# Optimization experiments

Measured on AMD Instinct MI355X. Metric: run time of the kernel, lower is better.

The kernel has to match this reference:

```python
import jax, jax.numpy as jnp
import numpy as np

B, N, E, H = 8, 1024, 768, 12
HD = E // H  # head_dim = 64
EPS = 1e-5


def setup_inputs() -> dict:
    key = jax.random.key(0)
    ks = jax.random.split(key, 3)
    x = jax.random.normal(ks[0], (B, N, E), dtype=jnp.float32)
    # Packed in-projection like torch nn.MultiheadAttention (in_proj_weight [3E, E])
    w_qkv = jax.random.normal(ks[1], (3 * E, E), dtype=jnp.float32) * (1.0 / np.sqrt(E))
    b_qkv = jnp.zeros((3 * E,), dtype=jnp.float32)
    w_out = jax.random.normal(ks[2], (E, E), dtype=jnp.float32) * (1.0 / np.sqrt(E))
    b_out = jnp.zeros((E,), dtype=jnp.float32)
    ln_g = jnp.ones((E,), dtype=jnp.float32)
    ln_b = jnp.zeros((E,), dtype=jnp.float32)
    return {"x": x, "ln_g": ln_g, "ln_b": ln_b, "w_qkv": w_qkv,
            "b_qkv": b_qkv, "w_out": w_out, "b_out": b_out}


def reference(x, ln_g, ln_b, w_qkv, b_qkv, w_out, b_out):
    # LayerNorm over last dim (eps=1e-5, elementwise affine)
    mu = jnp.mean(x, axis=-1, keepdims=True)
    var = jnp.mean(jnp.square(x - mu), axis=-1, keepdims=True)
    xn = (x - mu) * jax.lax.rsqrt(var + EPS) * ln_g + ln_b

    # Packed QKV projection: torch does x @ in_proj_weight.T + in_proj_bias
    qkv = jnp.einsum('bne,fe->bnf', xn, w_qkv) + b_qkv  # [B, N, 3E]
    q, k, v = jnp.split(qkv, 3, axis=-1)
    # Split heads -> [B, H, N, HD]
    q = q.reshape(B, N, H, HD).transpose(0, 2, 1, 3)
    k = k.reshape(B, N, H, HD).transpose(0, 2, 1, 3)
    v = v.reshape(B, N, H, HD).transpose(0, 2, 1, 3)

    scale = 1.0 / np.sqrt(HD)
    scores = jnp.einsum('bhqd,bhkd->bhqk', q * scale, k)  # [B, H, N, N]
    attn = jax.nn.softmax(scores, axis=-1)
    # (attn_dropout=0.0; need_weights=True forces this manual path in torch,
    #  averaged weights attn.mean(axis=1) are computed but not returned here
    #  since return_attention_map defaults to False)
    ctx = jnp.einsum('bhqk,bhkd->bhqd', attn, v)  # [B, H, N, HD]
    ctx = ctx.transpose(0, 2, 1, 3).reshape(B, N, E)

    out = jnp.einsum('bne,fe->bnf', ctx, w_out) + b_out  # out_proj
    return out
```

## Files before the change

kernel.cpp:

```cpp
#include <hip/hip_runtime.h>
#include <hip/hip_bf16.h>
#include <stdint.h>

#define B_ 8
#define N_ 1024
#define E_ 768
#define H_ 12
#define HD_ 64
#define M_ (B_ * N_)

typedef __attribute__((ext_vector_type(8))) short bf8_t;
typedef __attribute__((ext_vector_type(4))) float f4_t;
typedef __attribute__((ext_vector_type(16))) float f16_t;

__device__ __forceinline__ unsigned short f2bf(float f) {
  unsigned u = __builtin_bit_cast(unsigned, f);
  unsigned r = (u + 0x7fffu + ((u >> 16) & 1u)) >> 16;
  return (unsigned short)r;
}

__device__ __forceinline__ unsigned cvt_pk_bf16(float lo, float hi) {
  unsigned r;
  asm("v_cvt_pk_bf16_f32 %0, %1, %2" : "=v"(r) : "v"(lo), "v"(hi));
  return r;
}

__device__ __forceinline__ float exp2_hw(float x) {
  float r;
  asm("v_exp_f32 %0, %1" : "=v"(r) : "v"(x));
  return r;
}

__device__ __forceinline__ void load_lds16(const void* g, void* l) {
  __builtin_amdgcn_global_load_lds(
      (__attribute__((address_space(1))) void*)(g),
      (__attribute__((address_space(3))) void*)(l), 16, 0, 0);
}

#define WAITV(N)                                        \
  asm volatile("s_waitcnt vmcnt(" #N ")" ::: "memory"); \
  __builtin_amdgcn_sched_barrier(0);                    \
  __builtin_amdgcn_s_barrier();                         \
  __builtin_amdgcn_sched_barrier(0);

#define BAR2()                          \
  __builtin_amdgcn_sched_barrier(0);    \
  __builtin_amdgcn_s_barrier();         \
  __builtin_amdgcn_sched_barrier(0);

__device__ __forceinline__ int swz(int row) {
  return ((row ^ (row >> 3)) & 7) << 3;
}

#define F3(a, b, c) fmaxf(fmaxf((a), (b)), (c))

__global__ void k_cast_bf16(const float* __restrict__ in,
                            unsigned short* __restrict__ out, int n4) {
  int i = blockIdx.x * blockDim.x + threadIdx.x;
  if (i < n4) {
    float4 v = ((const float4*)in)[i];
    ushort4 o;
    o.x = f2bf(v.x); o.y = f2bf(v.y); o.z = f2bf(v.z); o.w = f2bf(v.w);
    ((ushort4*)out)[i] = o;
  }
}

__global__ __launch_bounds__(192) void k_ln(const float* __restrict__ x,
                                            const float* __restrict__ g,
                                            const float* __restrict__ bta,
                                            unsigned short* __restrict__ xn) {
  int row = blockIdx.x;
  int t = threadIdx.x;
  float4 v = ((const float4*)(x + (size_t)row * E_))[t];
  float s = v.x + v.y + v.z + v.w;
  float s2 = v.x * v.x + v.y * v.y + v.z * v.z + v.w * v.w;
  for (int off = 32; off; off >>= 1) {
    s += __shfl_xor(s, off, 64);
    s2 += __shfl_xor(s2, off, 64);
  }
  __shared__ float red[6];
  int lane = t & 63, wv = t >> 6;
  if (lane == 0) { red[wv] = s; red[3 + wv] = s2; }
  __syncthreads();
  s = red[0] + red[1] + red[2];
  s2 = red[3] + red[4] + red[5];
  float mu = s * (1.0f / E_);
  float var = s2 * (1.0f / E_) - mu * mu;
  float rstd = rsqrtf(var + 1e-5f);
  float4 gg = ((const float4*)g)[t];
  float4 bb = ((const float4*)bta)[t];
  ushort4 o;
  o.x = f2bf((v.x - mu) * rstd * gg.x + bb.x);
  o.y = f2bf((v.y - mu) * rstd * gg.y + bb.y);
  o.z = f2bf((v.z - mu) * rstd * gg.z + bb.z);
  o.w = f2bf((v.w - mu) * rstd * gg.w + bb.w);
  ((ushort4*)(xn + (size_t)row * E_))[t] = o;
}

template <int EPI>
__global__ __launch_bounds__(256) void k_gemm_bt(
    const unsigned short* __restrict__ A,
    const unsigned short* __restrict__ W,
    const float* __restrict__ bias,
    unsigned short* __restrict__ oQ, unsigned short* __restrict__ oK,
    unsigned short* __restrict__ oVt, float* __restrict__ oF,
    int K, int Nf) {
  __shared__ unsigned short Al[2][128 * 64];
  __shared__ unsigned short Bl[2][128 * 64];
  const int nbx = Nf >> 7;
  const int nwg = nbx << 6;
  const int orig = blockIdx.y * nbx + blockIdx.x;
  const int id = (orig & 7) * (nwg >> 3) + (orig >> 3);
  const int n0 = (id % nbx) * 128, m0 = (id / nbx) * 128;
  const int tid = threadIdx.x;
  const int lane = tid & 63, wv = tid >> 6;
  const int wr = wv >> 1, wc = wv & 1;
  const int g = lane >> 4, l15 = lane & 15;
  f4_t acc[4][4] = {};

  auto stage = [&](int k0, int buf) {
#pragma unroll
    for (int i = 0; i < 4; ++i) {
      int e = (i * 256 + tid) * 8;
      int r = e >> 6;
      int c = (e & 63) ^ swz(r);
      load_lds16(A + (size_t)(m0 + r) * K + (k0 + c), &Al[buf][e]);
      load_lds16(W + (size_t)(n0 + r) * K + (k0 + c), &Bl[buf][e]);
    }
  };

  stage(0, 0);
  __syncthreads();
  int cur = 0;

  for (int k0 = 0; k0 < K; k0 += 64) {
    if (k0 + 64 < K) stage(k0 + 64, cur ^ 1);
    const unsigned short* Ac = Al[cur];
    const unsigned short* Bc = Bl[cur];
#pragma unroll
    for (int kk = 0; kk < 2; ++kk) {
      bf8_t af[4], bfr[4];
#pragma unroll
      for (int mi = 0; mi < 4; ++mi) {
        int ar = wr * 64 + mi * 16 + l15;
        af[mi] = *(const bf8_t*)&Ac[(ar * 64 + kk * 32 + g * 8) ^ swz(ar)];
      }
#pragma unroll
      for (int ni = 0; ni < 4; ++ni) {
        int br = wc * 64 + ni * 16 + l15;
        bfr[ni] = *(const bf8_t*)&Bc[(br * 64 + kk * 32 + g * 8) ^ swz(br)];
      }
#pragma unroll
      for (int mi = 0; mi < 4; ++mi)
#pragma unroll
        for (int ni = 0; ni < 4; ++ni)
          acc[mi][ni] = __builtin_amdgcn_mfma_f32_16x16x32_bf16(
              af[mi], bfr[ni], acc[mi][ni], 0, 0, 0);
    }
    __syncthreads();
    cur ^= 1;
  }

#pragma unroll
  for (int mi = 0; mi < 4; ++mi) {
#pragma unroll
    for (int ni = 0; ni < 4; ++ni) {
      int f = n0 + wc * 64 + ni * 16 + l15;
      float bs = bias[f];
#pragma unroll
      for (int i = 0; i < 4; ++i) {
        int m = m0 + wr * 64 + mi * 16 + g * 4 + i;
        float val = acc[mi][ni][i] + bs;
        if (EPI == 0) {
          int bb = m >> 10, n = m & 1023;
          int which = f / E_;
          int e2 = f - which * E_;
          int h = e2 >> 6, d = e2 & 63;
          size_t qk = (((size_t)bb * H_ + h) * N_ + n) * HD_ + d;
          if (which == 0) oQ[qk] = f2bf(val * 0.1803368801f);
          else if (which == 1) oK[qk] = f2bf(val);
          else oVt[(((size_t)bb * H_ + h) * HD_ + d) * N_ + n] = f2bf(val);
        } else {
          oF[(size_t)m * E_ + f] = val;
        }
      }
    }
  }
}

__global__ __launch_bounds__(256, 3) void k_attn(
    const unsigned short* __restrict__ Q,
    const unsigned short* __restrict__ Kb,
    const unsigned short* __restrict__ Vt,
    unsigned short* __restrict__ ctx) {
  __shared__ unsigned short Kl[2][64 * 64];
  __shared__ unsigned short Vl[2][64 * 64];
  const int bh = blockIdx.x;
  const int qt = blockIdx.y;
  const int tid = threadIdx.x;
  const int lane = tid & 63, wv = tid >> 6;
  const int q5 = lane & 31, hi = lane >> 5;

  const unsigned short* Qp =
      Q + ((size_t)bh * N_ + qt * 128 + wv * 32 + q5) * HD_;
  bf8_t qf[4];
#pragma unroll
  for (int s = 0; s < 4; ++s)
    qf[s] = *(const bf8_t*)&Qp[s * 16 + hi * 8];

  f16_t o0 = {}, o1 = {};
  float mrow = -1e30f, lrow = 0.f;
  const unsigned short* Kbase = Kb + (size_t)bh * N_ * HD_;
  const unsigned short* Vbase = Vt + (size_t)bh * HD_ * N_;

  auto stage = [&](int t, int buf) {
#pragma unroll
    for (int i = 0; i < 2; ++i) {
      int e = (i * 256 + tid) * 8;
      int r = e >> 6;
      int c = (e & 63) ^ swz(r);
      load_lds16(Kbase + (size_t)(t * 64 + r) * HD_ + c, &Kl[buf][e]);
      load_lds16(Vbase + (size_t)r * N_ + (t * 64 + c), &Vl[buf][e]);
    }
  };

  stage(0, 0);
  stage(1, 1);

  for (int t = 0; t < 16; ++t) {
    const int cur = t & 1;
    if (t + 1 < 16) { WAITV(4); } else { WAITV(0); }
    const unsigned short* Klc = Kl[cur];
    const unsigned short* Vlc = Vl[cur];

    f16_t s0 = {}, s1 = {};
    __builtin_amdgcn_s_setprio(1);
#pragma unroll
    for (int s = 0; s < 4; ++s) {
      int doff = s * 16 + hi * 8;
      bf8_t k0 = *(const bf8_t*)&Klc[(q5 * 64 + doff) ^ swz(q5)];
      bf8_t k1 = *(const bf8_t*)&Klc[((32 + q5) * 64 + doff) ^ swz(32 + q5)];
      s0 = __builtin_amdgcn_mfma_f32_32x32x16_bf16(k0, qf[s], s0, 0, 0, 0);
      s1 = __builtin_amdgcn_mfma_f32_32x32x16_bf16(k1, qf[s], s1, 0, 0, 0);
    }
    __builtin_amdgcn_s_setprio(0);

    float v0 = F3(s0[0], s0[1], s0[2]),   v1 = F3(s0[3], s0[4], s0[5]);
    float v2 = F3(s0[6], s0[7], s0[8]),   v3 = F3(s0[9], s0[10], s0[11]);
    float v4 = F3(s0[12], s0[13], s0[14]), v5 = F3(s0[15], s1[0], s1[1]);
    float v6 = F3(s1[2], s1[3], s1[4]),   v7 = F3(s1[5], s1[6], s1[7]);
    float v8 = F3(s1[8], s1[9], s1[10]),  v9 = F3(s1[11], s1[12], s1[13]);
    float w0 = F3(v0, v1, v2), w1 = F3(v3, v4, v5);
    float w2 = F3(v6, v7, v8), w3 = F3(v9, s1[14], s1[15]);
    float mx = fmaxf(F3(w0, w1, w2), w3);

    if (!__all(mx - mrow <= 8.0f)) {
      float Mx = fmaxf(mx, __shfl_xor(mx, 32, 64));
      float mnew = fmaxf(mrow, Mx);
      float al = exp2_hw(mrow - mnew);
      lrow *= al;
#pragma unroll
      for (int r = 0; r < 16; ++r) { o0[r] *= al; o1[r] *= al; }
      mrow = mnew;
    }

    float p[32];
#pragma unroll
    for (int r = 0; r < 16; ++r) p[r] = exp2_hw(s0[r] - mrow);
#pragma unroll
    for (int r = 0; r < 16; ++r) p[16 + r] = exp2_hw(s1[r] - mrow);
    float acc0 = 0.f, acc1 = 0.f, acc2 = 0.f, acc3 = 0.f;
#pragma unroll
    for (int r = 0; r < 8; ++r) {
      acc0 += p[r]; acc1 += p[8 + r]; acc2 += p[16 + r]; acc3 += p[24 + r];
    }
    lrow += (acc0 + acc1) + (acc2 + acc3);

    unsigned pj[4][4];
#pragma unroll
    for (int s = 0; s < 4; ++s) {
      unsigned Ax = cvt_pk_bf16(p[8 * s + 0], p[8 * s + 1]);
      unsigned Cx = cvt_pk_bf16(p[8 * s + 2], p[8 * s + 3]);
      unsigned Ex = cvt_pk_bf16(p[8 * s + 4], p[8 * s + 5]);
      unsigned Fx = cvt_pk_bf16(p[8 * s + 6], p[8 * s + 7]);
      asm volatile("v_permlane32_swap_b32 %0, %1" : "+v"(Ax), "+v"(Ex));
      asm volatile("v_permlane32_swap_b32 %0, %1" : "+v"(Cx), "+v"(Fx));
      pj[s][0] = Ax; pj[s][1] = Cx; pj[s][2] = Ex; pj[s][3] = Fx;
    }

    __builtin_amdgcn_s_setprio(1);
#pragma unroll
    for (int s = 0; s < 4; ++s) {
      int koff = s * 16 + hi * 8;
      bf8_t pb;
      *(uint4*)&pb = *(uint4*)&pj[s][0];
      bf8_t vv0 = *(const bf8_t*)&Vlc[(q5 * 64 + koff) ^ swz(q5)];
      bf8_t vv1 = *(const bf8_t*)&Vlc[((32 + q5) * 64 + koff) ^ swz(32 + q5)];
      o0 = __builtin_amdgcn_mfma_f32_32x32x16_bf16(vv0, pb, o0, 0, 0, 0);
      o1 = __builtin_amdgcn_mfma_f32_32x32x16_bf16(vv1, pb, o1, 0, 0, 0);
    }
    __builtin_amdgcn_s_setprio(0);

    BAR2();
    if (t + 2 < 16) stage(t + 2, cur);
  }

  lrow += __shfl_xor(lrow, 32, 64);
  float rinv = 1.0f / lrow;

  unsigned short* Ol = &Kl[0][0] + wv * 2048;
#pragma unroll
  for (int f = 0; f < 2; ++f) {
#pragma unroll
    for (int r = 0; r < 16; r += 2) {
      int d = (r & 3) + 8 * (r >> 2) + 4 * hi + 32 * f;
      float lo = (f ? o1[r] : o0[r]) * rinv;
      float hi2 = (f ? o1[r + 1] : o0[r + 1]) * rinv;
      unsigned pk = cvt_pk_bf16(lo, hi2);
      *(unsigned*)&Ol[q5 * 64 + (d ^ ((q5 & 7) << 3))] = pk;
    }
  }
  asm volatile("s_waitcnt lgkmcnt(0)" ::: "memory");
  __builtin_amdgcn_sched_barrier(0);

  const int bb = bh / H_, h = bh - bb * H_;
  const int qq = lane >> 1;
#pragma unroll
  for (int k = 0; k < 4; ++k) {
    int c = (lane & 1) * 4 + k;
    bf8_t val = *(const bf8_t*)&Ol[qq * 64 + ((c * 8) ^ ((qq & 7) << 3))];
    unsigned short* dst = ctx +
        ((size_t)bb * N_ + qt * 128 + wv * 32 + qq) * E_ + h * HD_ + c * 8;
    *(bf8_t*)dst = val;
  }
}

extern "C" void kernel_launch(void* const* d_in, const int* in_sizes, int n_in,
                              void* d_out, int out_size, void* d_ws, size_t ws_size,
                              hipStream_t stream) {
  const float* x     = (const float*)d_in[0];
  const float* ln_g  = (const float*)d_in[1];
  const float* ln_b  = (const float*)d_in[2];
  const float* w_qkv = (const float*)d_in[3];
  const float* b_qkv = (const float*)d_in[4];
  const float* w_out = (const float*)d_in[5];
  const float* b_out = (const float*)d_in[6];
  float* out = (float*)d_out;

  char* ws = (char*)d_ws;
  const size_t SZ = (size_t)M_ * E_ * 2;
  unsigned short* xn    = (unsigned short*)(ws);
  unsigned short* qb    = (unsigned short*)(ws + SZ);
  unsigned short* kbuf  = (unsigned short*)(ws + 2 * SZ);
  unsigned short* vtb   = (unsigned short*)(ws + 3 * SZ);
  unsigned short* ctx   = (unsigned short*)(ws + 4 * SZ);
  unsigned short* wqkvb = (unsigned short*)(ws + 5 * SZ);
  unsigned short* woutb = (unsigned short*)(ws + 5 * SZ + (size_t)3 * E_ * E_ * 2);

  int n1 = 3 * E_ * E_ / 4;
  k_cast_bf16<<<(n1 + 255) / 256, 256, 0, stream>>>(w_qkv, wqkvb, n1);
  int n2 = E_ * E_ / 4;
  k_cast_bf16<<<(n2 + 255) / 256, 256, 0, stream>>>(w_out, woutb, n2);

  k_ln<<<M_, 192, 0, stream>>>(x, ln_g, ln_b, xn);

  k_gemm_bt<0><<<dim3(18, 64), 256, 0, stream>>>(xn, wqkvb, b_qkv, qb, kbuf, vtb,
                                                 nullptr, E_, 3 * E_);
  k_attn<<<dim3(96, 8), 256, 0, stream>>>(qb, kbuf, vtb, ctx);
  k_gemm_bt<1><<<dim3(6, 64), 256, 0, stream>>>(ctx, woutb, b_out, nullptr, nullptr,
                                                nullptr, out, E_, E_);
}
```

Measured before the change: 137.6 us.

## Use 256x128 GEMM tiles with 512 threads and triple-buffered LDS pipeline

Both projection GEMMs now use 512-thread workgroups covering 256x128 output tiles, with a three-stage LDS ring buffer. Wait counts on the vector memory counter replace full syncthreads, so loads stay two stages ahead of the MFMA work. MFMA sections are wrapped in raised wave priority. This aims to hide global-load latency and reuse each staged W tile across more rows. In exchange it uses much more LDS (about 144KB) and limits occupancy to one block per CU. It also halves the grid, which hurts the 6x32 out-projection launch in particular.

```diff
diff --git a/kernel.cpp b/kernel.cpp
--- a/kernel.cpp
+++ b/kernel.cpp
@@ -98,20 +98,20 @@
 }
 
 template <int EPI>
-__global__ __launch_bounds__(256) void k_gemm_bt(
+__global__ __launch_bounds__(512, 1) void k_gemm_deep(
     const unsigned short* __restrict__ A,
     const unsigned short* __restrict__ W,
     const float* __restrict__ bias,
     unsigned short* __restrict__ oQ, unsigned short* __restrict__ oK,
-    unsigned short* __restrict__ oVt, float* __restrict__ oF,
-    int K, int Nf) {
-  __shared__ unsigned short Al[2][128 * 64];
-  __shared__ unsigned short Bl[2][128 * 64];
+    unsigned short* __restrict__ oVt, float* __restrict__ oF, int Nf) {
+  __shared__ unsigned short Al[3][256 * 64];
+  __shared__ unsigned short Bl[3][128 * 64];
+  const int K = 768;
   const int nbx = Nf >> 7;
-  const int nwg = nbx << 6;
+  const int nwg = nbx << 5;
   const int orig = blockIdx.y * nbx + blockIdx.x;
   const int id = (orig & 7) * (nwg >> 3) + (orig >> 3);
-  const int n0 = (id % nbx) * 128, m0 = (id / nbx) * 128;
+  const int n0 = (id % nbx) * 128, m0 = (id / nbx) * 256;
   const int tid = threadIdx.x;
   const int lane = tid & 63, wv = tid >> 6;
   const int wr = wv >> 1, wc = wv & 1;
@@ -121,20 +121,29 @@
   auto stage = [&](int k0, int buf) {
 #pragma unroll
     for (int i = 0; i < 4; ++i) {
-      int e = (i * 256 + tid) * 8;
+      int e = (i * 512 + tid) * 8;
       int r = e >> 6;
       int c = (e & 63) ^ swz(r);
       load_lds16(A + (size_t)(m0 + r) * K + (k0 + c), &Al[buf][e]);
+    }
+#pragma unroll
+    for (int i = 0; i < 2; ++i) {
+      int e = (i * 512 + tid) * 8;
+      int r = e >> 6;
+      int c = (e & 63) ^ swz(r);
       load_lds16(W + (size_t)(n0 + r) * K + (k0 + c), &Bl[buf][e]);
     }
   };
 
   stage(0, 0);
-  __syncthreads();
-  int cur = 0;
-
-  for (int k0 = 0; k0 < K; k0 += 64) {
-    if (k0 + 64 < K) stage(k0 + 64, cur ^ 1);
+  stage(64, 1);
+  stage(128, 2);
+
+  for (int t = 0; t < 12; ++t) {
+    const int cur = t % 3;
+    if (t + 2 < 12)      { WAITV(12); }
+    else if (t + 1 < 12) { WAITV(6); }
+    else                 { WAITV(0); }
     const unsigned short* Ac = Al[cur];
     const unsigned short* Bc = Bl[cur];
 #pragma unroll
@@ -150,15 +159,17 @@
         int br = wc * 64 + ni * 16 + l15;
         bfr[ni] = *(const bf8_t*)&Bc[(br * 64 + kk * 32 + g * 8) ^ swz(br)];
       }
+      __builtin_amdgcn_s_setprio(1);
 #pragma unroll
       for (int mi = 0; mi < 4; ++mi)
 #pragma unroll
         for (int ni = 0; ni < 4; ++ni)
           acc[mi][ni] = __builtin_amdgcn_mfma_f32_16x16x32_bf16(
               af[mi], bfr[ni], acc[mi][ni], 0, 0, 0);
-    }
-    __syncthreads();
-    cur ^= 1;
+      __builtin_amdgcn_s_setprio(0);
+    }
+    BAR2();
+    if (t + 3 < 12) stage((t + 3) << 6, cur);
   }
 
 #pragma unroll
@@ -364,9 +375,9 @@
 
   k_ln<<<M_, 192, 0, stream>>>(x, ln_g, ln_b, xn);
 
-  k_gemm_bt<0><<<dim3(18, 64), 256, 0, stream>>>(xn, wqkvb, b_qkv, qb, kbuf, vtb,
-                                                 nullptr, E_, 3 * E_);
+  k_gemm_deep<0><<<dim3(18, 32), 512, 0, stream>>>(xn, wqkvb, b_qkv, qb, kbuf,
+                                                   vtb, nullptr, 3 * E_);
   k_attn<<<dim3(96, 8), 256, 0, stream>>>(qb, kbuf, vtb, ctx);
-  k_gemm_bt<1><<<dim3(6, 64), 256, 0, stream>>>(ctx, woutb, b_out, nullptr, nullptr,
-                                                nullptr, out, E_, E_);
-}
+  k_gemm_deep<1><<<dim3(6, 32), 512, 0, stream>>>(ctx, woutb, b_out, nullptr,
+                                                  nullptr, nullptr, out, E_);
+}
```

Measured after the change: 152.5 us. 1.11x slower.
